# Optimization experiments

Hardware: AMD Instinct MI355X
Metric: run time of the kernel (lower is better)

Reference implementation:

```python
import jax, jax.numpy as jnp
import numpy as np

B, NQ, NK, D, H = 4, 512, 512, 128, 32  # batch, n_queries, n_keys, kq_size, mlp hidden


def setup_inputs() -> dict:
    key = jax.random.key(0)
    ks = jax.random.split(key, 7)
    s_in = 1.0 / np.sqrt(2 * D)
    s_h = 1.0 / np.sqrt(H)
    return {
        "keys": jax.random.normal(ks[0], (B, NK, D), dtype=jnp.float32),
        "queries": jax.random.normal(ks[1], (B, NQ, D), dtype=jnp.float32),
        # first MLP layer Linear(2D, H) split into key-half and query-half
        "Wk": jax.random.uniform(ks[2], (D, H), jnp.float32, -s_in, s_in),
        "Wq": jax.random.uniform(ks[3], (D, H), jnp.float32, -s_in, s_in),
        "b1": jax.random.uniform(ks[4], (H,), jnp.float32, -s_in, s_in),
        # second MLP layer Linear(H, 1)
        "w2": jax.random.uniform(ks[5], (H,), jnp.float32, -s_h, s_h),
        "b2": jax.random.uniform(ks[6], (), jnp.float32, -s_h, s_h),
    }


def reference(keys, queries, Wk, Wq, b1, w2, b2):
    # AdditiveScorer: logits[b,q,k] = w2 . tanh(W1 @ [keys[b,k]; queries[b,q]] + b1) + b2
    # Split the concat-linear into two GEMMs (identical math, no [B,Q,K,2D] tensor).
    kh = jnp.einsum("bkd,dh->bkh", keys, Wk)            # (B, NK, H)
    qh = jnp.einsum("bqd,dh->bqh", queries, Wq)          # (B, NQ, H)
    h = jnp.tanh(qh[:, :, None, :] + kh[:, None, :, :] + b1)  # (B, NQ, NK, H)
    logits = jnp.einsum("bqkh,h->bqk", h, w2) + b2       # (B, NQ, NK)
    attn = jax.nn.softmax(logits, axis=-1)               # softmax over keys
    context = jnp.einsum("bqk,bkd->bqd", attn, keys)     # weighted value sum (values = keys)
    return context
```

## Files before the change

### kernel.cpp

```cpp
#include <hip/hip_runtime.h>

#define B 4
#define NQ 512
#define NK 512
#define D 128
#define H 32
#define G 4
#define PS 2.8853900817779268f

__device__ __forceinline__ float rcp_f(float x)  { return __builtin_amdgcn_rcpf(x); }
__device__ __forceinline__ float exp2_f(float x) { return __builtin_amdgcn_exp2f(x); }

__device__ __forceinline__ void fma4(float4& a, const float4& v, float s) {
    a.x = fmaf(s, v.x, a.x);
    a.y = fmaf(s, v.y, a.y);
    a.z = fmaf(s, v.z, a.z);
    a.w = fmaf(s, v.w, a.w);
}

__global__ __launch_bounds__(256) void proj_kernel(
    const float* __restrict__ keys, const float* __restrict__ queries,
    const float* __restrict__ Wk, const float* __restrict__ Wq,
    const float* __restrict__ b1,
    float* __restrict__ Ek, float* __restrict__ eq)
{
    __shared__ float xs[8][D];
    const int tid = threadIdx.x;
    const int r0 = blockIdx.x * 8;
    const bool is_q = (r0 >= B * NK);
    const float* __restrict__ X = is_q ? (queries + (size_t)(r0 - B * NK) * D)
                                       : (keys + (size_t)r0 * D);
    const float* __restrict__ W = is_q ? Wq : Wk;

    reinterpret_cast<float4*>(&xs[0][0])[tid] =
        reinterpret_cast<const float4*>(X)[tid];
    __syncthreads();

    const int lr = tid >> 5;
    const int h  = tid & 31;
    float a0 = 0.f, a1 = 0.f, a2 = 0.f, a3 = 0.f;
    const float4* x4 = reinterpret_cast<const float4*>(&xs[lr][0]);
    #pragma unroll
    for (int i = 0; i < D / 4; ++i) {
        float4 v = x4[i];
        a0 = fmaf(v.x, W[(4 * i + 0) * H + h], a0);
        a1 = fmaf(v.y, W[(4 * i + 1) * H + h], a1);
        a2 = fmaf(v.z, W[(4 * i + 2) * H + h], a2);
        a3 = fmaf(v.w, W[(4 * i + 3) * H + h], a3);
    }
    float acc = (a0 + a1) + (a2 + a3);
    if (is_q) {
        const int rq = r0 - B * NK + lr;
        eq[(size_t)rq * H + h] = exp2_f(acc * PS);
    } else {
        const int r = r0 + lr;
        const int b = r >> 9;
        const int k = r & (NK - 1);
        Ek[((size_t)b * H + h) * NK + k] = exp2_f((acc + b1[h]) * PS);
    }
}

__global__ __launch_bounds__(256) void attend_kernel(
    const float* __restrict__ keys,
    const float* __restrict__ Ek,
    const float* __restrict__ eq,
    const float* __restrict__ w2,
    float* __restrict__ outp)
{
    __shared__ float ex_t[G][NK];
    __shared__ float acc_s[8][G][D];
    __shared__ float eq_s[G][H];
    __shared__ float w2_s[H];

    const int tid  = threadIdx.x;
    const int lane = tid & 63;
    const int w    = tid >> 6;
    const int b    = blockIdx.x >> 7;
    const int q0   = (blockIdx.x & 127) * G;

    if (lane < H) {
        eq_s[w][lane] = eq[((size_t)b * NQ + q0 + w) * H + lane];
        if (w == 0) w2_s[lane] = -PS * w2[lane];
    }
    __syncthreads();

    float l[8];
    #pragma unroll
    for (int j = 0; j < 8; ++j) l[j] = 0.f;
    const float* Ekb = Ek + (size_t)b * H * NK;
    #pragma unroll 8
    for (int h = 0; h < H; ++h) {
        const float4 v0 = reinterpret_cast<const float4*>(Ekb + h * NK)[lane];
        const float4 v1 = reinterpret_cast<const float4*>(Ekb + h * NK + 256)[lane];
        const float ev = eq_s[w][h];
        const float wp = w2_s[h];
        l[0] = fmaf(wp, rcp_f(fmaf(ev, v0.x, 1.f)), l[0]);
        l[1] = fmaf(wp, rcp_f(fmaf(ev, v0.y, 1.f)), l[1]);
        l[2] = fmaf(wp, rcp_f(fmaf(ev, v0.z, 1.f)), l[2]);
        l[3] = fmaf(wp, rcp_f(fmaf(ev, v0.w, 1.f)), l[3]);
        l[4] = fmaf(wp, rcp_f(fmaf(ev, v1.x, 1.f)), l[4]);
        l[5] = fmaf(wp, rcp_f(fmaf(ev, v1.y, 1.f)), l[5]);
        l[6] = fmaf(wp, rcp_f(fmaf(ev, v1.z, 1.f)), l[6]);
        l[7] = fmaf(wp, rcp_f(fmaf(ev, v1.w, 1.f)), l[7]);
    }

    float m = l[0];
    #pragma unroll
    for (int j = 1; j < 8; ++j) m = fmaxf(m, l[j]);
    #pragma unroll
    for (int off = 32; off; off >>= 1) m = fmaxf(m, __shfl_xor(m, off));
    float e[8], s = 0.f;
    #pragma unroll
    for (int j = 0; j < 8; ++j) { e[j] = exp2_f(l[j] - m); s += e[j]; }
    #pragma unroll
    for (int off = 32; off; off >>= 1) s += __shfl_xor(s, off);
    const float inv = 1.f / s;
    const float4 st0 = { e[0] * inv, e[1] * inv, e[2] * inv, e[3] * inv };
    const float4 st1 = { e[4] * inv, e[5] * inv, e[6] * inv, e[7] * inv };
    reinterpret_cast<float4*>(&ex_t[w][0])[lane]   = st0;
    reinterpret_cast<float4*>(&ex_t[w][256])[lane] = st1;
    __syncthreads();

    const int dg = tid & 31;
    const int kp = tid >> 5;
    const float4* k4 = reinterpret_cast<const float4*>(
        keys + ((size_t)b * NK + kp * 64) * D) + dg;
    const float4* e0p = reinterpret_cast<const float4*>(&ex_t[0][kp * 64]);
    const float4* e1p = reinterpret_cast<const float4*>(&ex_t[1][kp * 64]);
    const float4* e2p = reinterpret_cast<const float4*>(&ex_t[2][kp * 64]);
    const float4* e3p = reinterpret_cast<const float4*>(&ex_t[3][kp * 64]);
    float4 a0 = {0,0,0,0}, a1 = a0, a2 = a0, a3 = a0;
    #pragma unroll 4
    for (int kk4 = 0; kk4 < 16; ++kk4) {
        float ea[4], eb[4], ec[4], ed[4];
        *reinterpret_cast<float4*>(ea) = e0p[kk4];
        *reinterpret_cast<float4*>(eb) = e1p[kk4];
        *reinterpret_cast<float4*>(ec) = e2p[kk4];
        *reinterpret_cast<float4*>(ed) = e3p[kk4];
        #pragma unroll
        for (int j = 0; j < 4; ++j) {
            float4 kv = k4[(size_t)(4 * kk4 + j) * (D / 4)];
            fma4(a0, kv, ea[j]);
            fma4(a1, kv, eb[j]);
            fma4(a2, kv, ec[j]);
            fma4(a3, kv, ed[j]);
        }
    }
    *reinterpret_cast<float4*>(&acc_s[kp][0][4 * dg]) = a0;
    *reinterpret_cast<float4*>(&acc_s[kp][1][4 * dg]) = a1;
    *reinterpret_cast<float4*>(&acc_s[kp][2][4 * dg]) = a2;
    *reinterpret_cast<float4*>(&acc_s[kp][3][4 * dg]) = a3;
    __syncthreads();

    const int o = 2 * tid;
    const int g = o >> 7;
    const int d = o & 127;
    float2 r = {0.f, 0.f};
    #pragma unroll
    for (int p = 0; p < 8; ++p) {
        float2 v = *reinterpret_cast<const float2*>(&acc_s[p][g][d]);
        r.x += v.x; r.y += v.y;
    }
    *reinterpret_cast<float2*>(&outp[((size_t)b * NQ + q0 + g) * D + d]) = r;
}

extern "C" void kernel_launch(void* const* d_in, const int* in_sizes, int n_in,
                              void* d_out, int out_size, void* d_ws, size_t ws_size,
                              hipStream_t stream) {
    const float* keys    = (const float*)d_in[0];
    const float* queries = (const float*)d_in[1];
    const float* Wk      = (const float*)d_in[2];
    const float* Wq      = (const float*)d_in[3];
    const float* b1      = (const float*)d_in[4];
    const float* w2      = (const float*)d_in[5];
    float* out = (float*)d_out;

    float* Ek = (float*)d_ws;
    float* eq = Ek + (size_t)B * H * NK;

    const int proj_blocks = (B * NK + B * NQ) / 8;
    proj_kernel<<<proj_blocks, 256, 0, stream>>>(keys, queries, Wk, Wq, b1, Ek, eq);
    attend_kernel<<<B * NQ / G, 256, 0, stream>>>(keys, Ek, eq, w2, out);
}
```

Before: 21.39 us.

## Double attend block to 512 threads, splitting logit keys and context reduction

The attend kernel now runs 512 threads per block. Eight waves each compute logits for half of the keys of one query, and the partial logits are staged in shared memory so four waves can do the softmax. The context accumulation splits keys into 16 partitions of 32 instead of 8 of 64, with a wider shared-memory reduction at the end. The aim is more parallelism and latency hiding per block while the grid size stays the same, at the cost of an extra barrier and shared-memory round trip, more LDS use, and idle waves during the softmax.

```diff
diff --git a/kernel.cpp b/kernel.cpp
--- a/kernel.cpp
+++ b/kernel.cpp
@@ -60,78 +60,88 @@
     }
 }
 
-__global__ __launch_bounds__(256) void attend_kernel(
+__global__ __launch_bounds__(512) void attend_kernel(
     const float* __restrict__ keys,
     const float* __restrict__ Ek,
     const float* __restrict__ eq,
     const float* __restrict__ w2,
     float* __restrict__ outp)
 {
+    __shared__ float lp[8][256];
     __shared__ float ex_t[G][NK];
-    __shared__ float acc_s[8][G][D];
+    __shared__ float acc_s[16][G][D];
     __shared__ float eq_s[G][H];
     __shared__ float w2_s[H];
 
     const int tid  = threadIdx.x;
     const int lane = tid & 63;
     const int w    = tid >> 6;
+    const int qw   = w & 3;
+    const int half = w >> 2;
     const int b    = blockIdx.x >> 7;
     const int q0   = (blockIdx.x & 127) * G;
 
     if (lane < H) {
-        eq_s[w][lane] = eq[((size_t)b * NQ + q0 + w) * H + lane];
-        if (w == 0) w2_s[lane] = -PS * w2[lane];
+        if (w < 4)  eq_s[w][lane] = eq[((size_t)b * NQ + q0 + w) * H + lane];
+        if (w == 4) w2_s[lane] = -PS * w2[lane];
     }
     __syncthreads();
 
-    float l[8];
-    #pragma unroll
-    for (int j = 0; j < 8; ++j) l[j] = 0.f;
-    const float* Ekb = Ek + (size_t)b * H * NK;
+    float l0 = 0.f, l1 = 0.f, l2 = 0.f, l3 = 0.f;
+    const float* Ekb = Ek + (size_t)b * H * NK + half * 256;
     #pragma unroll 8
     for (int h = 0; h < H; ++h) {
-        const float4 v0 = reinterpret_cast<const float4*>(Ekb + h * NK)[lane];
-        const float4 v1 = reinterpret_cast<const float4*>(Ekb + h * NK + 256)[lane];
-        const float ev = eq_s[w][h];
+        const float4 v = reinterpret_cast<const float4*>(Ekb + h * NK)[lane];
+        const float ev = eq_s[qw][h];
         const float wp = w2_s[h];
-        l[0] = fmaf(wp, rcp_f(fmaf(ev, v0.x, 1.f)), l[0]);
-        l[1] = fmaf(wp, rcp_f(fmaf(ev, v0.y, 1.f)), l[1]);
-        l[2] = fmaf(wp, rcp_f(fmaf(ev, v0.z, 1.f)), l[2]);
-        l[3] = fmaf(wp, rcp_f(fmaf(ev, v0.w, 1.f)), l[3]);
-        l[4] = fmaf(wp, rcp_f(fmaf(ev, v1.x, 1.f)), l[4]);
-        l[5] = fmaf(wp, rcp_f(fmaf(ev, v1.y, 1.f)), l[5]);
-        l[6] = fmaf(wp, rcp_f(fmaf(ev, v1.z, 1.f)), l[6]);
-        l[7] = fmaf(wp, rcp_f(fmaf(ev, v1.w, 1.f)), l[7]);
+        l0 = fmaf(wp, rcp_f(fmaf(ev, v.x, 1.f)), l0);
+        l1 = fmaf(wp, rcp_f(fmaf(ev, v.y, 1.f)), l1);
+        l2 = fmaf(wp, rcp_f(fmaf(ev, v.z, 1.f)), l2);
+        l3 = fmaf(wp, rcp_f(fmaf(ev, v.w, 1.f)), l3);
     }
+    {
+        const float4 st = { l0, l1, l2, l3 };
+        reinterpret_cast<float4*>(&lp[w][0])[lane] = st;
+    }
+    __syncthreads();
 
-    float m = l[0];
-    #pragma unroll
-    for (int j = 1; j < 8; ++j) m = fmaxf(m, l[j]);
-    #pragma unroll
-    for (int off = 32; off; off >>= 1) m = fmaxf(m, __shfl_xor(m, off));
-    float e[8], s = 0.f;
-    #pragma unroll
-    for (int j = 0; j < 8; ++j) { e[j] = exp2_f(l[j] - m); s += e[j]; }
-    #pragma unroll
-    for (int off = 32; off; off >>= 1) s += __shfl_xor(s, off);
-    const float inv = 1.f / s;
-    const float4 st0 = { e[0] * inv, e[1] * inv, e[2] * inv, e[3] * inv };
-    const float4 st1 = { e[4] * inv, e[5] * inv, e[6] * inv, e[7] * inv };
-    reinterpret_cast<float4*>(&ex_t[w][0])[lane]   = st0;
-    reinterpret_cast<float4*>(&ex_t[w][256])[lane] = st1;
+    if (w < 4) {
+        float l[8];
+        {
+            const float4 L0 = reinterpret_cast<const float4*>(&lp[w][0])[lane];
+            const float4 L1 = reinterpret_cast<const float4*>(&lp[w + 4][0])[lane];
+            l[0] = L0.x; l[1] = L0.y; l[2] = L0.z; l[3] = L0.w;
+            l[4] = L1.x; l[5] = L1.y; l[6] = L1.z; l[7] = L1.w;
+        }
+        float m = l[0];
+        #pragma unroll
+        for (int j = 1; j < 8; ++j) m = fmaxf(m, l[j]);
+        #pragma unroll
+        for (int off = 32; off; off >>= 1) m = fmaxf(m, __shfl_xor(m, off));
+        float e[8], s = 0.f;
+        #pragma unroll
+        for (int j = 0; j < 8; ++j) { e[j] = exp2_f(l[j] - m); s += e[j]; }
+        #pragma unroll
+        for (int off = 32; off; off >>= 1) s += __shfl_xor(s, off);
+        const float inv = 1.f / s;
+        const float4 st0 = { e[0] * inv, e[1] * inv, e[2] * inv, e[3] * inv };
+        const float4 st1 = { e[4] * inv, e[5] * inv, e[6] * inv, e[7] * inv };
+        reinterpret_cast<float4*>(&ex_t[w][0])[lane]   = st0;
+        reinterpret_cast<float4*>(&ex_t[w][256])[lane] = st1;
+    }
     __syncthreads();
 
     const int dg = tid & 31;
     const int kp = tid >> 5;
     const float4* k4 = reinterpret_cast<const float4*>(
-        keys + ((size_t)b * NK + kp * 64) * D) + dg;
-    const float4* e0p = reinterpret_cast<const float4*>(&ex_t[0][kp * 64]);
-    const float4* e1p = reinterpret_cast<const float4*>(&ex_t[1][kp * 64]);
-    const float4* e2p = reinterpret_cast<const float4*>(&ex_t[2][kp * 64]);
-    const float4* e3p = reinterpret_cast<const float4*>(&ex_t[3][kp * 64]);
+        keys + ((size_t)b * NK + kp * 32) * D) + dg;
+    const float4* e0p = reinterpret_cast<const float4*>(&ex_t[0][kp * 32]);
+    const float4* e1p = reinterpret_cast<const float4*>(&ex_t[1][kp * 32]);
+    const float4* e2p = reinterpret_cast<const float4*>(&ex_t[2][kp * 32]);
+    const float4* e3p = reinterpret_cast<const float4*>(&ex_t[3][kp * 32]);
     float4 a0 = {0,0,0,0}, a1 = a0, a2 = a0, a3 = a0;
-    #pragma unroll 4
-    for (int kk4 = 0; kk4 < 16; ++kk4) {
+    #pragma unroll 2
+    for (int kk4 = 0; kk4 < 8; ++kk4) {
         float ea[4], eb[4], ec[4], ed[4];
         *reinterpret_cast<float4*>(ea) = e0p[kk4];
         *reinterpret_cast<float4*>(eb) = e1p[kk4];
@@ -152,16 +162,12 @@
     *reinterpret_cast<float4*>(&acc_s[kp][3][4 * dg]) = a3;
     __syncthreads();
 
-    const int o = 2 * tid;
-    const int g = o >> 7;
-    const int d = o & 127;
-    float2 r = {0.f, 0.f};
+    const int g = tid >> 7;
+    const int d = tid & 127;
+    float r = 0.f;
     #pragma unroll
-    for (int p = 0; p < 8; ++p) {
-        float2 v = *reinterpret_cast<const float2*>(&acc_s[p][g][d]);
-        r.x += v.x; r.y += v.y;
-    }
-    *reinterpret_cast<float2*>(&outp[((size_t)b * NQ + q0 + g) * D + d]) = r;
+    for (int p = 0; p < 16; ++p) r += acc_s[p][g][d];
+    outp[((size_t)b * NQ + q0 + g) * D + d] = r;
 }
 
 extern "C" void kernel_launch(void* const* d_in, const int* in_sizes, int n_in,
@@ -180,5 +186,5 @@
 
     const int proj_blocks = (B * NK + B * NQ) / 8;
     proj_kernel<<<proj_blocks, 256, 0, stream>>>(keys, queries, Wk, Wq, b1, Ek, eq);
-    attend_kernel<<<B * NQ / G, 256, 0, stream>>>(keys, Ek, eq, w2, out);
+    attend_kernel<<<B * NQ / G, 512, 0, stream>>>(keys, Ek, eq, w2, out);
 }
```

After: 20.24 us. 1.06x faster.
